# Performance work log

Hardware: AMD Instinct MI355X
Metric: run time of the kernel (lower is better)

The kernel has to match this reference:

```python
import itertools
import jax, jax.numpy as jnp
import numpy as np

LATENT_DIM = 8
N = 2 * LATENT_DIM  # width of z_combined = concat([z, dz])
BATCH = 131072

# Static combinatorial index sets, matching the nested-loop order
# (i <= j [<= k]) of the torch implementation exactly.
_PAIRS = np.array(list(itertools.combinations_with_replacement(range(N), 2)), dtype=np.int32)   # [136, 2]
_TRIPLES = np.array(list(itertools.combinations_with_replacement(range(N), 3)), dtype=np.int32)  # [816, 3]


def setup_inputs() -> dict:
    key = jax.random.key(0)
    k1, k2 = jax.random.split(key)
    z = jax.random.normal(k1, (BATCH, LATENT_DIM), dtype=jnp.float32)
    dz = jax.random.normal(k2, (BATCH, LATENT_DIM), dtype=jnp.float32)
    return {"z": z, "dz": dz}


def reference(z, dz):
    # z, dz: [B, latent_dim] -> Theta: [B, 985]
    zc = jnp.concatenate([z, dz], axis=1)  # [B, N]
    B = zc.shape[0]
    ones = jnp.ones((B, 1), dtype=zc.dtype)
    # degree-2 terms: zc[:, i] * zc[:, j] for i <= j, all at once via gather
    deg2 = zc[:, _PAIRS[:, 0]] * zc[:, _PAIRS[:, 1]]  # [B, 136]
    # degree-3 terms: zc[:, i] * zc[:, j] * zc[:, k] for i <= j <= k
    deg3 = zc[:, _TRIPLES[:, 0]] * zc[:, _TRIPLES[:, 1]] * zc[:, _TRIPLES[:, 2]]  # [B, 816]
    sine = jnp.sin(zc)  # [B, N]
    return jnp.concatenate([ones, zc, deg2, deg3, sine], axis=1)  # [B, 985]
```

## Files before the change

### kernel.cpp

```cpp
#include <hip/hip_runtime.h>
#include <math.h>

#define NDIM   16
#define NPAIR  136
#define NTRIP  816
#define NCOL   985
#define GROUPS 8
#define ROWS_PER_BLOCK (4 * GROUPS)

__global__ __launch_bounds__(256) void sindy_kernel(
    const float* __restrict__ z, const float* __restrict__ dz,
    float* __restrict__ out, int batch)
{
    __shared__ unsigned short table[NPAIR + NTRIP];
    __shared__ float zbuf[4][NDIM];

    for (int e = threadIdx.x; e < NPAIR + NTRIP; e += blockDim.x) {
        unsigned short pk;
        if (e < NPAIR) {
            int p = e, i = 0;
            while (p >= NDIM - i) { p -= NDIM - i; ++i; }
            int j = i + p;
            pk = (unsigned short)(i | (j << 4));
        } else {
            int t = e - NPAIR, i = 0;
            for (;;) {
                int cnt = (NDIM - i) * (NDIM - i + 1) / 2;
                if (t < cnt) break;
                t -= cnt; ++i;
            }
            int j = i;
            while (t >= NDIM - j) { t -= NDIM - j; ++j; }
            int k = j + t;
            pk = (unsigned short)(i | (j << 4) | (k << 8));
        }
        table[e] = pk;
    }
    __syncthreads();

    const int wid  = threadIdx.x >> 6;
    const int lane = threadIdx.x & 63;

    const int row0 = blockIdx.x * ROWS_PER_BLOCK;
    for (int g = 0; g < GROUPS; ++g) {
        const int rowbase = row0 + g * 4;

        __syncthreads();
        if (threadIdx.x < 64) {
            int r = threadIdx.x >> 4;
            int c = threadIdx.x & 15;
            int row = rowbase + r;
            float v = 0.f;
            if (row < batch) v = (c < 8) ? z[row * 8 + c] : dz[row * 8 + (c - 8)];
            zbuf[r][c] = v;
        }
        __syncthreads();

        const int row = rowbase + wid;
        if (row < batch) {
            float* __restrict__ orow = out + (size_t)row * NCOL;
            const float* zr = zbuf[wid];
            #pragma unroll
            for (int it = 0; it < 16; ++it) {
                int col = it * 64 + lane;
                if (col < NCOL) {
                    float v;
                    if (col == 0) {
                        v = 1.0f;
                    } else if (col < 1 + NDIM) {
                        v = zr[col - 1];
                    } else if (col < 1 + NDIM + NPAIR) {
                        unsigned pk = table[col - (1 + NDIM)];
                        v = zr[pk & 15] * zr[(pk >> 4) & 15];
                    } else if (col < 1 + NDIM + NPAIR + NTRIP) {
                        unsigned pk = table[NPAIR + (col - (1 + NDIM + NPAIR))];
                        v = zr[pk & 15] * zr[(pk >> 4) & 15] * zr[(pk >> 8) & 15];
                    } else {
                        v = sinf(zr[col - (1 + NDIM + NPAIR + NTRIP)]);
                    }
                    orow[col] = v;
                }
            }
        }
    }
}

extern "C" void kernel_launch(void* const* d_in, const int* in_sizes, int n_in,
                              void* d_out, int out_size, void* d_ws, size_t ws_size,
                              hipStream_t stream) {
    const float* z  = (const float*)d_in[0];
    const float* dz = (const float*)d_in[1];
    float* out = (float*)d_out;
    const int batch = in_sizes[0] / 8;

    const int blocks = (batch + ROWS_PER_BLOCK - 1) / ROWS_PER_BLOCK;
    sindy_kernel<<<blocks, 256, 0, stream>>>(z, dz, out, batch);
}
```

Baseline: 129.1 us.

## Compute one row per lane with compile-time indices and transpose through shared slab

Each lane now owns a full row: it loads z/dz with float4 loads and computes every output term from registers, with term indices resolved at compile time through template expansion, so there is no shared index table. Results are written in chunks of 62 columns into a padded per-wave shared-memory slab and then transposed, so each store instruction writes contiguous columns of one row. The goal is to remove the index-table lookups, per-group block syncs and divergent branches. In exchange the code is much larger, the kernel uses about 63KB of shared memory per block (limiting occupancy), and sinf becomes the less accurate __sinf.

```diff
diff --git a/kernel.cpp b/kernel.cpp
--- a/kernel.cpp
+++ b/kernel.cpp
@@ -1,98 +1,108 @@
 #include <hip/hip_runtime.h>
-#include <math.h>
+#include <utility>
+#include <cstddef>
 
-#define NDIM   16
-#define NPAIR  136
-#define NTRIP  816
-#define NCOL   985
-#define GROUPS 8
-#define ROWS_PER_BLOCK (4 * GROUPS)
+#define NCOLS  985
+#define CHUNK  62
+#define NCHUNK 16
+#define PITCH  63
 
-__global__ __launch_bounds__(256) void sindy_kernel(
-    const float* __restrict__ z, const float* __restrict__ dz,
-    float* __restrict__ out, int batch)
-{
-    __shared__ unsigned short table[NPAIR + NTRIP];
-    __shared__ float zbuf[4][NDIM];
+constexpr int pair_i_f(int p){ int i=0; while (p >= 16-i){ p -= 16-i; ++i; } return i; }
+constexpr int pair_j_f(int p){ int i=0; while (p >= 16-i){ p -= 16-i; ++i; } return i+p; }
+constexpr int tcount(int i){ return (16-i)*(17-i)/2; }
+constexpr int trip_i_f(int t){ int i=0; while (t >= tcount(i)){ t -= tcount(i); ++i; } return i; }
+constexpr int trip_j_f(int t){ int i=0; while (t >= tcount(i)){ t -= tcount(i); ++i; }
+                               int j=i; while (t >= 16-j){ t -= 16-j; ++j; } return j; }
+constexpr int trip_k_f(int t){ int i=0; while (t >= tcount(i)){ t -= tcount(i); ++i; }
+                               int j=i; while (t >= 16-j){ t -= 16-j; ++j; } return j+t; }
 
-    for (int e = threadIdx.x; e < NPAIR + NTRIP; e += blockDim.x) {
-        unsigned short pk;
-        if (e < NPAIR) {
-            int p = e, i = 0;
-            while (p >= NDIM - i) { p -= NDIM - i; ++i; }
-            int j = i + p;
-            pk = (unsigned short)(i | (j << 4));
-        } else {
-            int t = e - NPAIR, i = 0;
-            for (;;) {
-                int cnt = (NDIM - i) * (NDIM - i + 1) / 2;
-                if (t < cnt) break;
-                t -= cnt; ++i;
-            }
-            int j = i;
-            while (t >= NDIM - j) { t -= NDIM - j; ++j; }
-            int k = j + t;
-            pk = (unsigned short)(i | (j << 4) | (k << 8));
-        }
-        table[e] = pk;
-    }
-    __syncthreads();
+template<int E>
+__device__ __forceinline__ float term(const float (&zc)[16]) {
+  if constexpr (E == 0) {
+    return 1.0f;
+  } else if constexpr (E <= 16) {
+    return zc[E-1];
+  } else if constexpr (E < 17 + 136) {
+    constexpr int p = E - 17;
+    constexpr int i = pair_i_f(p), j = pair_j_f(p);
+    return zc[i] * zc[j];
+  } else if constexpr (E < 17 + 136 + 816) {
+    constexpr int t = E - 153;
+    constexpr int i = trip_i_f(t), j = trip_j_f(t), k = trip_k_f(t);
+    return (zc[i] * zc[j]) * zc[k];
+  } else {
+    return __sinf(zc[E - 969]);
+  }
+}
 
-    const int wid  = threadIdx.x >> 6;
-    const int lane = threadIdx.x & 63;
+template<int BEG, int... Is>
+__device__ __forceinline__ void chunk_compute(const float (&zc)[16], float* sl,
+                                              std::integer_sequence<int, Is...>) {
+  ((sl[Is] = term<BEG + Is>(zc)), ...);
+}
 
-    const int row0 = blockIdx.x * ROWS_PER_BLOCK;
-    for (int g = 0; g < GROUPS; ++g) {
-        const int rowbase = row0 + g * 4;
+template<int C>
+__device__ __forceinline__ void do_chunk(const float (&zc)[16], float* sl, float* slw,
+                                         float* outbase, int lane, int nrows) {
+  constexpr int BEG = C * CHUNK;
+  constexpr int LEN = (BEG + CHUNK <= NCOLS) ? CHUNK : (NCOLS - BEG);
+  chunk_compute<BEG>(zc, sl, std::make_integer_sequence<int, LEN>{});
+  __builtin_amdgcn_sched_barrier(0);
+  float* op = outbase + BEG + lane;
+  #pragma unroll 8
+  for (int rr = 0; rr < 64; ++rr) {
+    float v = slw[rr * PITCH + lane];
+    if (lane < LEN && rr < nrows) op[(size_t)rr * NCOLS] = v;
+  }
+  __builtin_amdgcn_sched_barrier(0);
+}
 
-        __syncthreads();
-        if (threadIdx.x < 64) {
-            int r = threadIdx.x >> 4;
-            int c = threadIdx.x & 15;
-            int row = rowbase + r;
-            float v = 0.f;
-            if (row < batch) v = (c < 8) ? z[row * 8 + c] : dz[row * 8 + (c - 8)];
-            zbuf[r][c] = v;
-        }
-        __syncthreads();
+template<int... Cs>
+__device__ __forceinline__ void all_chunks(const float (&zc)[16], float* sl, float* slw,
+                                           float* outbase, int lane, int nrows,
+                                           std::integer_sequence<int, Cs...>) {
+  (do_chunk<Cs>(zc, sl, slw, outbase, lane, nrows), ...);
+}
 
-        const int row = rowbase + wid;
-        if (row < batch) {
-            float* __restrict__ orow = out + (size_t)row * NCOL;
-            const float* zr = zbuf[wid];
-            #pragma unroll
-            for (int it = 0; it < 16; ++it) {
-                int col = it * 64 + lane;
-                if (col < NCOL) {
-                    float v;
-                    if (col == 0) {
-                        v = 1.0f;
-                    } else if (col < 1 + NDIM) {
-                        v = zr[col - 1];
-                    } else if (col < 1 + NDIM + NPAIR) {
-                        unsigned pk = table[col - (1 + NDIM)];
-                        v = zr[pk & 15] * zr[(pk >> 4) & 15];
-                    } else if (col < 1 + NDIM + NPAIR + NTRIP) {
-                        unsigned pk = table[NPAIR + (col - (1 + NDIM + NPAIR))];
-                        v = zr[pk & 15] * zr[(pk >> 4) & 15] * zr[(pk >> 8) & 15];
-                    } else {
-                        v = sinf(zr[col - (1 + NDIM + NPAIR + NTRIP)]);
-                    }
-                    orow[col] = v;
-                }
-            }
-        }
-    }
+__global__ __launch_bounds__(256) void sindy_kernel(const float* __restrict__ z,
+                                                    const float* __restrict__ dz,
+                                                    float* __restrict__ out, int batch) {
+  __shared__ float slab[4][64 * PITCH];
+
+  const int w    = threadIdx.x >> 6;
+  const int lane = threadIdx.x & 63;
+  const int row0 = blockIdx.x * 256 + w * 64;
+  if (row0 >= batch) return;
+  const int nrows = (batch - row0 < 64) ? (batch - row0) : 64;
+
+  const int lrow = (row0 + lane < batch) ? (row0 + lane) : (batch - 1);
+  float zc[16];
+  {
+    const float4* zp = (const float4*)(z  + (size_t)lrow * 8);
+    const float4* dp = (const float4*)(dz + (size_t)lrow * 8);
+    float4 a = zp[0], b = zp[1], c = dp[0], d = dp[1];
+    zc[0]=a.x;  zc[1]=a.y;  zc[2]=a.z;  zc[3]=a.w;
+    zc[4]=b.x;  zc[5]=b.y;  zc[6]=b.z;  zc[7]=b.w;
+    zc[8]=c.x;  zc[9]=c.y;  zc[10]=c.z; zc[11]=c.w;
+    zc[12]=d.x; zc[13]=d.y; zc[14]=d.z; zc[15]=d.w;
+  }
+
+  float* slw = slab[w];
+  float* sl  = slw + lane * PITCH;
+  float* outbase = out + (size_t)row0 * NCOLS;
+
+  all_chunks(zc, sl, slw, outbase, lane, nrows,
+             std::make_integer_sequence<int, NCHUNK>{});
 }
 
 extern "C" void kernel_launch(void* const* d_in, const int* in_sizes, int n_in,
                               void* d_out, int out_size, void* d_ws, size_t ws_size,
                               hipStream_t stream) {
-    const float* z  = (const float*)d_in[0];
-    const float* dz = (const float*)d_in[1];
-    float* out = (float*)d_out;
-    const int batch = in_sizes[0] / 8;
+  const float* z  = (const float*)d_in[0];
+  const float* dz = (const float*)d_in[1];
+  float* out = (float*)d_out;
+  const int batch = in_sizes[0] / 8;
 
-    const int blocks = (batch + ROWS_PER_BLOCK - 1) / ROWS_PER_BLOCK;
-    sindy_kernel<<<blocks, 256, 0, stream>>>(z, dz, out, batch);
+  const int blocks = (batch + 255) / 256;
+  sindy_kernel<<<blocks, 256, 0, stream>>>(z, dz, out, batch);
 }
```

Result: slower. 228.7 us (+77.1%).

## Use per-wave row ownership and uniform table-driven products without block barriers

Applied to the files above, without the earlier changes.

Each wavefront now owns 16 consecutive rows and stages its own z row in a private LDS slot. This removes the two block-wide __syncthreads per row group. The index table is extended so the constant and linear columns are encoded as products with a padding slot holding 1.0, which gives the first 960 columns one branch-free path; sine switches to the fast __sinf intrinsic. The risks are reduced accuracy from __sinf and reliance on wave-level lockstep for the LDS write-then-read with no explicit barrier. Each block also covers twice as many rows, which halves the grid.

```diff
diff --git a/kernel.cpp b/kernel.cpp
--- a/kernel.cpp
+++ b/kernel.cpp
@@ -1,98 +1,86 @@
 #include <hip/hip_runtime.h>
-#include <math.h>
+#include <cstddef>
 
 #define NDIM   16
-#define NPAIR  136
-#define NTRIP  816
-#define NCOL   985
-#define GROUPS 8
-#define ROWS_PER_BLOCK (4 * GROUPS)
+#define NTAB   969
+#define NCOLS  985
+#define RPW    16
+#define SLOT   17
 
-__global__ __launch_bounds__(256) void sindy_kernel(
-    const float* __restrict__ z, const float* __restrict__ dz,
-    float* __restrict__ out, int batch)
-{
-    __shared__ unsigned short table[NPAIR + NTRIP];
-    __shared__ float zbuf[4][NDIM];
+__global__ __launch_bounds__(256) void sindy_kernel(const float* __restrict__ z,
+                                                    const float* __restrict__ dz,
+                                                    float* __restrict__ out, int batch) {
+  __shared__ unsigned short tab[NTAB];
+  __shared__ float zs[4][SLOT];
 
-    for (int e = threadIdx.x; e < NPAIR + NTRIP; e += blockDim.x) {
-        unsigned short pk;
-        if (e < NPAIR) {
-            int p = e, i = 0;
-            while (p >= NDIM - i) { p -= NDIM - i; ++i; }
-            int j = i + p;
-            pk = (unsigned short)(i | (j << 4));
-        } else {
-            int t = e - NPAIR, i = 0;
-            for (;;) {
-                int cnt = (NDIM - i) * (NDIM - i + 1) / 2;
-                if (t < cnt) break;
-                t -= cnt; ++i;
-            }
-            int j = i;
-            while (t >= NDIM - j) { t -= NDIM - j; ++j; }
-            int k = j + t;
-            pk = (unsigned short)(i | (j << 4) | (k << 8));
-        }
-        table[e] = pk;
+  for (int e = threadIdx.x; e < NTAB; e += 256) {
+    int i = 16, j = 16, k = 16;
+    if (e >= 1 && e <= 16) {
+      i = e - 1;
+    } else if (e >= 17 && e < 153) {
+      int p = e - 17; i = 0;
+      while (p >= 16 - i) { p -= 16 - i; ++i; }
+      j = i + p;
+    } else if (e >= 153) {
+      int t = e - 153; i = 0;
+      for (;;) { int c = (16 - i) * (17 - i) / 2; if (t < c) break; t -= c; ++i; }
+      j = i;
+      while (t >= 16 - j) { t -= 16 - j; ++j; }
+      k = j + t;
     }
-    __syncthreads();
+    tab[e] = (unsigned short)(i | (j << 5) | (k << 10));
+  }
+  __syncthreads();
 
-    const int wid  = threadIdx.x >> 6;
-    const int lane = threadIdx.x & 63;
+  const int w = threadIdx.x >> 6;
+  const int l = threadIdx.x & 63;
+  float* zr = zs[w];
 
-    const int row0 = blockIdx.x * ROWS_PER_BLOCK;
-    for (int g = 0; g < GROUPS; ++g) {
-        const int rowbase = row0 + g * 4;
+  const int rbase = (blockIdx.x * 4 + w) * RPW;
 
-        __syncthreads();
-        if (threadIdx.x < 64) {
-            int r = threadIdx.x >> 4;
-            int c = threadIdx.x & 15;
-            int row = rowbase + r;
-            float v = 0.f;
-            if (row < batch) v = (c < 8) ? z[row * 8 + c] : dz[row * 8 + (c - 8)];
-            zbuf[r][c] = v;
-        }
-        __syncthreads();
+  for (int rr = 0; rr < RPW; ++rr) {
+    const int row = rbase + rr;
+    if (row >= batch) break;
 
-        const int row = rowbase + wid;
-        if (row < batch) {
-            float* __restrict__ orow = out + (size_t)row * NCOL;
-            const float* zr = zbuf[wid];
-            #pragma unroll
-            for (int it = 0; it < 16; ++it) {
-                int col = it * 64 + lane;
-                if (col < NCOL) {
-                    float v;
-                    if (col == 0) {
-                        v = 1.0f;
-                    } else if (col < 1 + NDIM) {
-                        v = zr[col - 1];
-                    } else if (col < 1 + NDIM + NPAIR) {
-                        unsigned pk = table[col - (1 + NDIM)];
-                        v = zr[pk & 15] * zr[(pk >> 4) & 15];
-                    } else if (col < 1 + NDIM + NPAIR + NTRIP) {
-                        unsigned pk = table[NPAIR + (col - (1 + NDIM + NPAIR))];
-                        v = zr[pk & 15] * zr[(pk >> 4) & 15] * zr[(pk >> 8) & 15];
-                    } else {
-                        v = sinf(zr[col - (1 + NDIM + NPAIR + NTRIP)]);
-                    }
-                    orow[col] = v;
-                }
-            }
-        }
+    if (l < SLOT) {
+      float v = 1.0f;
+      if (l < 8)       v = z[(size_t)row * 8 + l];
+      else if (l < 16) v = dz[(size_t)row * 8 + (l - 8)];
+      zr[l] = v;
     }
+
+    float* orow = out + (size_t)row * NCOLS;
+
+    #pragma unroll
+    for (int it = 0; it < 15; ++it) {
+      const int col = it * 64 + l;
+      const unsigned pk = tab[col];
+      const float v = zr[pk & 31] * zr[(pk >> 5) & 31] * zr[(pk >> 10) & 31];
+      orow[col] = v;
+    }
+
+    if (l < NCOLS - 960) {
+      const int col = 960 + l;
+      float v;
+      if (col < NTAB) {
+        const unsigned pk = tab[col];
+        v = zr[pk & 31] * zr[(pk >> 5) & 31] * zr[(pk >> 10) & 31];
+      } else {
+        v = __sinf(zr[col - NTAB]);
+      }
+      orow[col] = v;
+    }
+  }
 }
 
 extern "C" void kernel_launch(void* const* d_in, const int* in_sizes, int n_in,
                               void* d_out, int out_size, void* d_ws, size_t ws_size,
                               hipStream_t stream) {
-    const float* z  = (const float*)d_in[0];
-    const float* dz = (const float*)d_in[1];
-    float* out = (float*)d_out;
-    const int batch = in_sizes[0] / 8;
+  const float* z  = (const float*)d_in[0];
+  const float* dz = (const float*)d_in[1];
+  float* out = (float*)d_out;
+  const int batch = in_sizes[0] / 8;
 
-    const int blocks = (batch + ROWS_PER_BLOCK - 1) / ROWS_PER_BLOCK;
-    sindy_kernel<<<blocks, 256, 0, stream>>>(z, dz, out, batch);
+  const int blocks = (batch + 4 * RPW - 1) / (4 * RPW);
+  sindy_kernel<<<blocks, 256, 0, stream>>>(z, dz, out, batch);
 }
```

Result: no change. 127.0 us (-1.6%).
